# Optimization experiments

Hardware: AMD Instinct MI355X
Metric: run time of the kernel (lower is better)

## Reference

```python
import jax, jax.numpy as jnp
import numpy as np

B, Q, H, W, C = 2, 8192, 64, 64, 64
C9 = C * 9
EPS = 1e-6


def _mlp(x, params):
    # gelu MLP, no activation on last layer (matches repo mlp)
    for Wm, b in params[:-1]:
        x = jax.nn.gelu(x @ Wm + b)
    Wl, bl = params[-1]
    return x @ Wl + bl


def _make_coord(h, w):
    # pixel-center coords in (-1,1); channel 0 = row dim, channel 1 = col dim
    hs = -1.0 + (2.0 * jnp.arange(h, dtype=jnp.float32) + 1.0) / h
    ws = -1.0 + (2.0 * jnp.arange(w, dtype=jnp.float32) + 1.0) / w
    return jnp.stack(jnp.meshgrid(hs, ws, indexing='ij'), axis=0)  # (2,h,w)


def _nearest_gather(feat, coord):
    # F.grid_sample(mode='nearest', align_corners=False) on a (B,1,q,2) grid.
    # feat (B,C,H,W); coord (B,q,2) with [...,0] indexing H, [...,1] indexing W
    h, w = feat.shape[-2], feat.shape[-1]
    ih = jnp.clip(jnp.round((coord[..., 0] + 1.0) * h / 2.0 - 0.5), 0, h - 1).astype(jnp.int32)
    iw = jnp.clip(jnp.round((coord[..., 1] + 1.0) * w / 2.0 - 0.5), 0, w - 1).astype(jnp.int32)
    return jax.vmap(lambda f, a, b: f[:, a, b].T)(feat, ih, iw)  # (B,q,C)


def _unfold3(feat):
    # F.unfold(feat, 3, padding=1).view(B, C*9, H, W): channel-major, kernel row-major
    b, c, h, w = feat.shape
    p = jnp.pad(feat, ((0, 0), (0, 0), (1, 1), (1, 1)))
    patches = jnp.stack([p[:, :, i:i + h, j:j + w] for i in range(3) for j in range(3)], axis=2)
    return patches.reshape(b, c * 9, h, w)


def _forward(inp, coord, scale, enc_w, enc_b, iw0, ib0, iw1, ib1, iw2, ib2,
             sw0, sb0, sw1, sb1, ww0, wb0, ww1, wb1):
    # encoder (stand-in conv3x3, 3 -> C feature channels)
    feat = jax.lax.conv_general_dilated(inp, enc_w, (1, 1), 'SAME',
                                        dimension_numbers=('NCHW', 'OIHW', 'NCHW'))
    feat = feat + enc_b[None, :, None, None]
    feat = _unfold3(feat)  # (B, C*9, H, W)
    bsz, cf, h, w = feat.shape
    fcoord = jnp.broadcast_to(_make_coord(h, w)[None], (bsz, 2, h, w))
    dims = jnp.array([h, w], dtype=feat.dtype)

    tx = (h - 1) / (1.0 - scale[:, 0, 0])  # (B,)
    ty = (w - 1) / (1.0 - scale[:, 0, 1])
    rx, ry = 1.0 / tx, 1.0 / ty
    scale_tok = scale * dims  # (B,q,2)

    imnet_p = [(iw0, ib0), (iw1, ib1), (iw2, ib2)]
    score_p = [(sw0, sb0), (sw1, sb1)]
    weight_p = [(ww0, wb0), (ww1, wb1)]

    preds = []
    for vx in (-1, 1):
        for vy in (-1, 1):
            shift = jnp.stack([vx * rx + EPS, vy * ry + EPS], axis=-1)[:, None, :]  # (B,1,2)
            c = jnp.clip(coord + shift, -1.0 + 1e-6, 1.0 - 1e-6)
            value = _nearest_gather(feat, c)      # (B,q,C*9)
            coord_k = _nearest_gather(fcoord, c)  # (B,q,2)
            rel = (coord - coord_k) * dims        # (B,q,2)
            score = _mlp(rel, score_p)            # (B,q,1) -> broadcast over 3
            mlp_in = jnp.concatenate([rel, scale_tok], axis=-1)  # (B,q,4)
            wmat = _mlp(mlp_in, imnet_p).reshape(bsz, -1, cf, 3)  # (B,q,C*9,3)
            preds.append(jnp.einsum('bqc,bqck->bqk', value, wmat) + score)
    stacked = jnp.stack(preds, axis=-1)  # (B,q,3,4)
    return _mlp(stacked, weight_p)[..., 0]  # (B,q,3)


def setup_inputs() -> dict:
    key = jax.random.key(0)
    ks = jax.random.split(key, 16)
    f32 = jnp.float32

    def wi(k, shape, fan_in):
        return jax.random.normal(k, shape, f32) / np.float32(np.sqrt(fan_in))

    return {
        'inp': jax.random.normal(ks[0], (B, 3, H, W), f32),
        'coord': jax.random.uniform(ks[1], (B, Q, 2), f32, -1.0 + 1e-4, 1.0 - 1e-4),
        'scale': jax.random.uniform(ks[2], (B, Q, 2), f32, 0.01, 0.05),
        'enc_w': wi(ks[3], (C, 3, 3, 3), 27),
        'enc_b': jnp.zeros((C,), f32),
        'iw0': wi(ks[4], (4, 256), 4), 'ib0': jnp.zeros((256,), f32),
        'iw1': wi(ks[5], (256, 256), 256), 'ib1': jnp.zeros((256,), f32),
        'iw2': wi(ks[6], (256, C9 * 3), 256), 'ib2': jnp.zeros((C9 * 3,), f32),
        'sw0': wi(ks[7], (2, 256), 2), 'sb0': jnp.zeros((256,), f32),
        'sw1': wi(ks[8], (256, 1), 256), 'sb1': jnp.zeros((1,), f32),
        'ww0': wi(ks[9], (4, 256), 4), 'wb0': jnp.zeros((256,), f32),
        'ww1': wi(ks[10], (256, 1), 256), 'wb1': jnp.zeros((1,), f32),
    }


def reference(inp, coord, scale, enc_w, enc_b, iw0, ib0, iw1, ib1, iw2, ib2,
              sw0, sb0, sw1, sb1, ww0, wb0, ww1, wb1):
    return _forward(inp, coord, scale, enc_w, enc_b, iw0, ib0, iw1, ib1, iw2, ib2,
                    sw0, sb0, sw1, sb1, ww0, wb0, ww1, wb1)
```

## Files before the change

### kernel.cpp

```cpp
#include <hip/hip_runtime.h>

#define QN 8192
#define CCH 64
#define NROW 65536
#define MR 64
#define NBLK (NROW / MR)
#define H0S 264

typedef _Float16 f16x8 __attribute__((ext_vector_type(8)));
typedef _Float16 f16x4 __attribute__((ext_vector_type(4)));
typedef float f32x4 __attribute__((ext_vector_type(4)));

__device__ __forceinline__ float gelu_f(float x) {
    float x2 = x * x;
    float tt = fmaf(0.044715f, x2, 1.0f);
    float e = __expf(1.5957691216f * x * tt);
    float r = __builtin_amdgcn_rcpf(1.0f + e);
    return x - x * r;
}

__global__ __launch_bounds__(256) void k_pre(const float* __restrict__ inp,
                                             const float* __restrict__ ew,
                                             const float* __restrict__ eb,
                                             const float* __restrict__ coord,
                                             const float* __restrict__ scale,
                                             const float* __restrict__ sw0,
                                             const float* __restrict__ sb0,
                                             const float* __restrict__ sw1,
                                             const float* __restrict__ sb1,
                                             const float* __restrict__ iw1,
                                             const float* __restrict__ iw2,
                                             const float* __restrict__ ib2,
                                             float* __restrict__ featpad,
                                             float4* __restrict__ mlp_in,
                                             int2* __restrict__ ihiw,
                                             float* __restrict__ scoreg,
                                             _Float16* __restrict__ w1tp,
                                             _Float16* __restrict__ w2tp,
                                             float* __restrict__ b2p) {
    const int bb = blockIdx.x;
    const int tt0 = threadIdx.x;
    if (bb < 2178) {
        __shared__ float s_ew[1728];
        for (int i = tt0; i < 1728; i += 256) s_ew[i] = ew[i];
        __syncthreads();
        int idx = bb * 256 + tt0;
        const int total = 2 * 66 * 66 * CCH;
        if (idx >= total) return;
        int o = idx & 63; int pix = idx >> 6;
        int xx = pix % 66; int t2 = pix / 66;
        int yy = t2 % 66;  int b = t2 / 66;
        int y = yy - 1, x = xx - 1;
        float acc = 0.0f;
        if (y >= 0 && y < 64 && x >= 0 && x < 64) {
            acc = eb[o];
            for (int i = 0; i < 3; ++i) {
                const float* ip = inp + ((b * 3 + i) * 64) * 64;
                const float* wp = s_ew + (o * 3 + i) * 9;
                #pragma unroll
                for (int ky = 0; ky < 3; ++ky) {
                    int sy = y + ky - 1;
                    if (sy < 0 || sy > 63) continue;
                    #pragma unroll
                    for (int kx = 0; kx < 3; ++kx) {
                        int sx = x + kx - 1;
                        if (sx < 0 || sx > 63) continue;
                        acc += ip[sy * 64 + sx] * wp[ky * 3 + kx];
                    }
                }
            }
        }
        featpad[idx] = acc;
    } else if (bb < 2434) {
        int row = (bb - 2178) * 256 + tt0;
        int v = row & 3;
        int bq = row >> 2;
        int b = bq >> 13;
        float c0 = coord[bq * 2 + 0], c1 = coord[bq * 2 + 1];
        float s0 = scale[bq * 2 + 0], s1 = scale[bq * 2 + 1];
        float s00 = scale[(b * QN) * 2 + 0];
        float s01 = scale[(b * QN) * 2 + 1];
        float rx = (1.0f - s00) / 63.0f;
        float ry = (1.0f - s01) / 63.0f;
        float vx = (v & 2) ? 1.0f : -1.0f;
        float vy = (v & 1) ? 1.0f : -1.0f;
        float cc0 = c0 + vx * rx + 1e-6f;
        float cc1 = c1 + vy * ry + 1e-6f;
        cc0 = fminf(fmaxf(cc0, -1.0f + 1e-6f), 1.0f - 1e-6f);
        cc1 = fminf(fmaxf(cc1, -1.0f + 1e-6f), 1.0f - 1e-6f);
        int ih = (int)rintf((cc0 + 1.0f) * 32.0f - 0.5f);
        int iw = (int)rintf((cc1 + 1.0f) * 32.0f - 0.5f);
        ih = min(max(ih, 0), 63);
        iw = min(max(iw, 0), 63);
        float ck0 = (2.0f * (float)ih + 1.0f) / 64.0f - 1.0f;
        float ck1 = (2.0f * (float)iw + 1.0f) / 64.0f - 1.0f;
        float rel0 = (c0 - ck0) * 64.0f;
        float rel1 = (c1 - ck1) * 64.0f;
        mlp_in[row] = make_float4(rel0, rel1, s0 * 64.0f, s1 * 64.0f);
        ihiw[row] = make_int2(ih, iw);
        float sc = sb1[0];
        #pragma unroll 4
        for (int t2 = 0; t2 < 256; ++t2) {
            float h = gelu_f(fmaf(rel0, sw0[t2], fmaf(rel1, sw0[256 + t2], sb0[t2])));
            sc = fmaf(h, sw1[t2], sc);
        }
        scoreg[row] = sc;
    } else {
        int idx = (bb - 2434) * 256 + tt0;
        if (idx < 442368) {
            int j = idx & 7, ln = (idx >> 3) & 63, kf = (idx >> 9) & 7, tl = idx >> 12;
            int np = tl * 16 + (ln & 15);
            int kk = kf * 32 + (ln >> 4) * 8 + j;
            int k_out = np / 576;
            int rem = np - 576 * k_out;
            int tap = rem >> 6, cch = rem & 63;
            int n = (cch * 9 + tap) * 3 + k_out;
            w2tp[idx] = (_Float16)iw2[kk * 1728 + n];
            if (kf == 0 && j == 0 && (ln >> 4) == 0) b2p[np] = ib2[n];
        } else {
            int i2 = idx - 442368;
            int j = i2 & 7, ln = (i2 >> 3) & 63, kf = (i2 >> 9) & 7, ct = i2 >> 12;
            int col = ct * 16 + (ln & 15);
            int kk = kf * 32 + (ln >> 4) * 8 + j;
            w1tp[i2] = (_Float16)iw1[kk * 256 + col];
        }
    }
}

#define LDX1(B, CT) do { const _Float16* wp_ = w1tp + (size_t)((CT) * 8) * 512 + lane * 8;        \
    _Pragma("unroll") for (int kf_ = 0; kf_ < 4; ++kf_) B[kf_] = *(const f16x8*)(wp_ + kf_ * 512); } while (0)
#define LDY1(B, CT) do { const _Float16* wp_ = w1tp + (size_t)((CT) * 8 + 4) * 512 + lane * 8;    \
    _Pragma("unroll") for (int kf_ = 0; kf_ < 4; ++kf_) B[kf_] = *(const f16x8*)(wp_ + kf_ * 512); } while (0)
#define LDX2(B, TI) do { const _Float16* wp_ = w2tp + (size_t)((TI) * 8) * 512 + lane * 8;        \
    _Pragma("unroll") for (int kf_ = 0; kf_ < 4; ++kf_) B[kf_] = *(const f16x8*)(wp_ + kf_ * 512); } while (0)
#define LDY2(B, BV, TI) do { const _Float16* wp_ = w2tp + (size_t)((TI) * 8 + 4) * 512 + lane * 8;\
    _Pragma("unroll") for (int kf_ = 0; kf_ < 4; ++kf_) B[kf_] = *(const f16x8*)(wp_ + kf_ * 512);\
    BV = b2p[(TI) * 16 + l15]; } while (0)
#define ZACCB(BV) do { _Pragma("unroll") for (int rt_ = 0; rt_ < 4; ++rt_)                        \
    acc[rt_] = (f32x4){(BV), (BV), (BV), (BV)}; } while (0)
#define MFMAH(B, OFS) do { _Pragma("unroll") for (int kf_ = 0; kf_ < 4; ++kf_)                    \
    { _Pragma("unroll") for (int rt_ = 0; rt_ < 4; ++rt_)                                         \
      acc[rt_] = __builtin_amdgcn_mfma_f32_16x16x32_f16(a[rt_][kf_ + (OFS)], B[kf_], acc[rt_], 0, 0, 0); } } while (0)
#define H1EPI(CT) do { int col_ = (CT) * 16 + l15;                                                \
    _Pragma("unroll") for (int rt_ = 0; rt_ < 4; ++rt_)                                           \
      { _Pragma("unroll") for (int rg_ = 0; rg_ < 4; ++rg_)                                       \
        s_h0[(rt_ * 16 + quad * 4 + rg_) * H0S + col_] = (_Float16)gelu_f(acc[rt_][rg_]); } } while (0)
#define VLD(TI) do { int cf36_ = (TI) - ((TI) / 36) * 36;                                         \
    const _Float16* vb_ = s_valT + (cf36_ * 16 + l15) * 64;                                       \
    vv0 = *(const f16x4*)(vb_ + ((0  + quad * 4) ^ swz));                                         \
    vv1 = *(const f16x4*)(vb_ + ((16 + quad * 4) ^ swz));                                         \
    vv2 = *(const f16x4*)(vb_ + ((32 + quad * 4) ^ swz));                                         \
    vv3 = *(const f16x4*)(vb_ + ((48 + quad * 4) ^ swz)); } while (0)
#define EPIR(RT, VV) do { _Pragma("unroll") for (int rg_ = 0; rg_ < 4; ++rg_)                     \
    pA[RT][rg_] = fmaf(acc[RT][rg_], (float)VV[rg_], pA[RT][rg_]); } while (0)
#define EPI3F() do { EPIR(0, vv0); EPIR(1, vv1); EPIR(2, vv2); EPIR(3, vv3); } while (0)
#define FLUSH(KT) do { _Pragma("unroll") for (int rt_ = 0; rt_ < 4; ++rt_)                        \
    { _Pragma("unroll") for (int rg_ = 0; rg_ < 4; ++rg_) {                                       \
        float x_ = pA[rt_][rg_];                                                                  \
        _Pragma("unroll") for (int m_ = 1; m_ < 16; m_ <<= 1) x_ += __shfl_xor(x_, m_, 64);       \
        if (l15 == 0) atomicAdd(&s_pred[rt_ * 16 + quad * 4 + rg_][KT], x_);                      \
        pA[rt_][rg_] = 0.f; } } } while (0)

__global__ __launch_bounds__(256, 2) void k_fused(const float* __restrict__ featpad,
                                                  const float4* __restrict__ mlp_in,
                                                  const int2* __restrict__ ihiw,
                                                  const float* __restrict__ iw0,
                                                  const float* __restrict__ ib0,
                                                  const _Float16* __restrict__ w1tp,
                                                  const float* __restrict__ ib1,
                                                  const _Float16* __restrict__ w2tp,
                                                  const float* __restrict__ b2p,
                                                  const float* __restrict__ scoreg,
                                                  const float* __restrict__ ww0,
                                                  const float* __restrict__ wb0,
                                                  const float* __restrict__ ww1,
                                                  const float* __restrict__ wb1,
                                                  float* __restrict__ out) {
    __shared__ __align__(16) char pool[576 * 64 * 2];
    _Float16* s_h0   = (_Float16*)pool;
    _Float16* s_valT = (_Float16*)pool;
    __shared__ float4 s_min[MR];
    __shared__ int    s_base[MR];
    __shared__ int    s_dtab[9];
    __shared__ float  s_pred[MR][3];
    __shared__ float  s_score[MR];
    __shared__ float  s_wred[48][4];

    const int t = threadIdx.x;
    const int wave = t >> 6, lane = t & 63, quad = lane >> 4, l15 = lane & 15;
    const int rowbase = blockIdx.x * MR;

    if (t < MR) {
        int row = rowbase + t;
        s_min[t] = mlp_in[row];
        s_score[t] = scoreg[row];
        int b = row >> 15;
        int2 p = ihiw[row];
        s_base[t] = ((b * 66 + p.x) * 66 + p.y) * 64;
    }
    if (t < 9) { int di = t / 3; s_dtab[t] = (di * 66 + (t - 3 * di)) * 64; }
    if (t < MR * 3) s_pred[t / 3][t % 3] = 0.0f;
    __syncthreads();

    {
        float w0 = iw0[t], w1 = iw0[256 + t], w2 = iw0[512 + t], w3 = iw0[768 + t];
        float bb = ib0[t];
        #pragma unroll 4
        for (int r = 0; r < MR; ++r) {
            float4 m = s_min[r];
            s_h0[r * H0S + t] =
                (_Float16)gelu_f(fmaf(m.x, w0, fmaf(m.y, w1, fmaf(m.z, w2, fmaf(m.w, w3, bb)))));
        }
    }
    __syncthreads();

    const int w4 = wave * 4;
    const int tbase = wave * 27;

    const float bibA = ib1[(w4 + 0) * 16 + l15];
    const float bibB = ib1[(w4 + 1) * 16 + l15];
    const float bibC = ib1[(w4 + 2) * 16 + l15];
    const float bibD = ib1[(w4 + 3) * 16 + l15];

    f16x8 bX0[4], bX1[4], bY0[4], bY1[4];
    float bv0, bv1;
    f32x4 acc[4];

    LDX1(bX0, w4);
    LDY1(bY0, w4);
    LDX1(bX1, w4 + 1);

    f16x8 a[4][8];
    #pragma unroll
    for (int rt = 0; rt < 4; ++rt)
        #pragma unroll
        for (int kf = 0; kf < 8; ++kf)
            a[rt][kf] = *(const f16x8*)(s_h0 + (rt * 16 + l15) * H0S + kf * 32 + quad * 8);
    __syncthreads();

    LDY1(bY1, w4 + 1);
    ZACCB(bibA); MFMAH(bX0, 0);
    LDX1(bX0, w4 + 2);
    MFMAH(bY0, 4);
    H1EPI(w4);
    LDY1(bY0, w4 + 2);
    ZACCB(bibB); MFMAH(bX1, 0);
    LDX1(bX1, w4 + 3);
    MFMAH(bY1, 4);
    H1EPI(w4 + 1);
    LDY1(bY1, w4 + 3);
    ZACCB(bibC); MFMAH(bX0, 0);
    LDX2(bX0, tbase);
    MFMAH(bY0, 4);
    H1EPI(w4 + 2);
    LDY2(bY0, bv0, tbase);
    ZACCB(bibD); MFMAH(bX1, 0);
    LDX2(bX1, tbase + 1);
    MFMAH(bY1, 4);
    H1EPI(w4 + 3);
    __syncthreads();

    #pragma unroll
    for (int rt = 0; rt < 4; ++rt)
        #pragma unroll
        for (int kf = 0; kf < 8; ++kf)
            a[rt][kf] = *(const f16x8*)(s_h0 + (rt * 16 + l15) * H0S + kf * 32 + quad * 8);
    __syncthreads();

    #pragma unroll 1
    for (int g4 = 0; g4 < 9; ++g4) {
        float4 v[4];
        #pragma unroll
        for (int u = 0; u < 4; ++u) {
            int c4 = wave + (g4 * 4 + u) * 4;
            int tap = c4 >> 4;
            int cch0 = (c4 & 15) << 2;
            v[u] = *(const float4*)(featpad + s_base[lane] + s_dtab[tap] + cch0);
        }
        #pragma unroll
        for (int u = 0; u < 4; ++u) {
            int c4 = wave + (g4 * 4 + u) * 4;
            int cfp = c4 << 2;
            s_valT[(cfp + 0) * 64 + (lane ^ (((cfp + 0) & 7) << 3))] = (_Float16)v[u].x;
            s_valT[(cfp + 1) * 64 + (lane ^ (((cfp + 1) & 7) << 3))] = (_Float16)v[u].y;
            s_valT[(cfp + 2) * 64 + (lane ^ (((cfp + 2) & 7) << 3))] = (_Float16)v[u].z;
            s_valT[(cfp + 3) * 64 + (lane ^ (((cfp + 3) & 7) << 3))] = (_Float16)v[u].w;
        }
    }
    __syncthreads();

    const int kt0 = tbase / 36;
    int bsplit = (kt0 + 1) * 36 - tbase; if (bsplit > 27) bsplit = 27;
    const int ktB = (tbase + 26) / 36;
    const int swz = (l15 & 7) << 3;

    f16x4 vv0, vv1, vv2, vv3;
    float pA[4][4];
    #pragma unroll
    for (int rt = 0; rt < 4; ++rt)
        #pragma unroll
        for (int rg = 0; rg < 4; ++rg) pA[rt][rg] = 0.f;

    #pragma unroll 1
    for (int p = 0; p < 13; ++p) {
        int i = 2 * p;
        int ti = tbase + i;
        LDY2(bY1, bv1, ti + 1);
        VLD(ti);
        ZACCB(bv0); MFMAH(bX0, 0);
        LDX2(bX0, ti + 2);
        MFMAH(bY0, 4);
        EPI3F();
        if (i == bsplit - 1) FLUSH(kt0);
        LDY2(bY0, bv0, ti + 2);
        VLD(ti + 1);
        ZACCB(bv1); MFMAH(bX1, 0);
        if (p < 12) LDX2(bX1, ti + 3);
        MFMAH(bY1, 4);
        EPI3F();
        if (i + 1 == bsplit - 1) FLUSH(kt0);
    }
    {
        VLD(tbase + 26);
        ZACCB(bv0); MFMAH(bX0, 0); MFMAH(bY0, 4);
        EPI3F();
        if (26 == bsplit - 1) FLUSH(kt0);
    }
    FLUSH(ktB);
    __syncthreads();

    if (t < 192) {
        int o = t >> 2, sub = t & 3;
        int bql = o / 3, k = o - 3 * bql;
        float x0 = s_pred[bql * 4 + 0][k] + s_score[bql * 4 + 0];
        float x1 = s_pred[bql * 4 + 1][k] + s_score[bql * 4 + 1];
        float x2 = s_pred[bql * 4 + 2][k] + s_score[bql * 4 + 2];
        float x3 = s_pred[bql * 4 + 3][k] + s_score[bql * 4 + 3];
        float acc2 = 0.0f;
        int j0 = sub * 64;
        #pragma unroll 4
        for (int j = j0; j < j0 + 64; ++j) {
            float h = gelu_f(fmaf(x0, ww0[j], fmaf(x1, ww0[256 + j],
                          fmaf(x2, ww0[512 + j], fmaf(x3, ww0[768 + j], wb0[j])))));
            acc2 = fmaf(h, ww1[j], acc2);
        }
        s_wred[o][sub] = acc2;
    }
    __syncthreads();
    if (t < 48) {
        int bql = t / 3, k = t - 3 * bql;
        float r2 = s_wred[t][0] + s_wred[t][1] + s_wred[t][2] + s_wred[t][3] + wb1[0];
        out[(blockIdx.x * 16 + bql) * 3 + k] = r2;
    }
}

extern "C" void kernel_launch(void* const* d_in, const int* in_sizes, int n_in,
                              void* d_out, int out_size, void* d_ws, size_t ws_size,
                              hipStream_t stream) {
    const float* inp   = (const float*)d_in[0];
    const float* coord = (const float*)d_in[1];
    const float* scale = (const float*)d_in[2];
    const float* ew    = (const float*)d_in[3];
    const float* eb    = (const float*)d_in[4];
    const float* iw0   = (const float*)d_in[5];
    const float* ib0   = (const float*)d_in[6];
    const float* iw1   = (const float*)d_in[7];
    const float* ib1   = (const float*)d_in[8];
    const float* iw2   = (const float*)d_in[9];
    const float* ib2   = (const float*)d_in[10];
    const float* sw0   = (const float*)d_in[11];
    const float* sb0   = (const float*)d_in[12];
    const float* sw1   = (const float*)d_in[13];
    const float* sb1   = (const float*)d_in[14];
    const float* ww0   = (const float*)d_in[15];
    const float* wb0   = (const float*)d_in[16];
    const float* ww1   = (const float*)d_in[17];
    const float* wb1   = (const float*)d_in[18];
    float* out = (float*)d_out;

    char* ws = (char*)d_ws;
    float*     featpad = (float*)(ws + 0);
    float4*    mlp_in  = (float4*)(ws + 2230272);
    int2*      ihiw    = (int2*)(ws + 3278848);
    float*     scoreg  = (float*)(ws + 3803136);
    _Float16*  w1tp    = (_Float16*)(ws + 4065280);
    _Float16*  w2tp    = (_Float16*)(ws + 4196352);
    float*     b2p     = (float*)(ws + 5081088);

    k_pre<<<dim3(4418), dim3(256), 0, stream>>>(inp, ew, eb, coord, scale,
                                                sw0, sb0, sw1, sb1, iw1, iw2, ib2,
                                                featpad, mlp_in, ihiw, scoreg,
                                                w1tp, w2tp, b2p);
    k_fused<<<dim3(NBLK), dim3(256), 0, stream>>>(featpad, mlp_in, ihiw,
                                                  iw0, ib0, w1tp, ib1, w2tp, b2p,
                                                  scoreg, ww0, wb0, ww1, wb1, out);
}
```

Measured before the change: 240.7 us.

## Software-pipeline feature gather, raise MFMA wave priority, use exp2 in gelu

Replaces the 9-iteration gather loop with a double-buffered sequence of 8-wide float4 loads into two register sets, so global loads overlap the LDS transpose stores. The first gather batch is also issued before the A-fragment reload. Each MFMA burst is wrapped in s_setprio so waves issuing matrix ops get scheduling priority over epilogue waves. The value reads from s_valT move from before the MFMAs to inside the epilogue, which shortens register live ranges. gelu now calls the native exp2 with a folded log2(e) constant. The cost is more registers for the 16 float4 buffers, which could hurt occupancy at launch_bounds(256,2).

```diff
diff --git a/kernel.cpp b/kernel.cpp
--- a/kernel.cpp
+++ b/kernel.cpp
@@ -14,7 +14,7 @@
 __device__ __forceinline__ float gelu_f(float x) {
     float x2 = x * x;
     float tt = fmaf(0.044715f, x2, 1.0f);
-    float e = __expf(1.5957691216f * x * tt);
+    float e = __builtin_amdgcn_exp2f(2.3022081597f * x * tt);
     float r = __builtin_amdgcn_rcpf(1.0f + e);
     return x - x * r;
 }
@@ -145,21 +145,31 @@
     _Pragma("unroll") for (int rt_ = 0; rt_ < 4; ++rt_)                                           \
       { _Pragma("unroll") for (int rg_ = 0; rg_ < 4; ++rg_)                                       \
         s_h0[(rt_ * 16 + quad * 4 + rg_) * H0S + col_] = (_Float16)gelu_f(acc[rt_][rg_]); } } while (0)
-#define VLD(TI) do { int cf36_ = (TI) - ((TI) / 36) * 36;                                         \
+#define EPI3(TI) do { int cf36_ = (TI) - ((TI) / 36) * 36;                                        \
     const _Float16* vb_ = s_valT + (cf36_ * 16 + l15) * 64;                                       \
-    vv0 = *(const f16x4*)(vb_ + ((0  + quad * 4) ^ swz));                                         \
-    vv1 = *(const f16x4*)(vb_ + ((16 + quad * 4) ^ swz));                                         \
-    vv2 = *(const f16x4*)(vb_ + ((32 + quad * 4) ^ swz));                                         \
-    vv3 = *(const f16x4*)(vb_ + ((48 + quad * 4) ^ swz)); } while (0)
-#define EPIR(RT, VV) do { _Pragma("unroll") for (int rg_ = 0; rg_ < 4; ++rg_)                     \
-    pA[RT][rg_] = fmaf(acc[RT][rg_], (float)VV[rg_], pA[RT][rg_]); } while (0)
-#define EPI3F() do { EPIR(0, vv0); EPIR(1, vv1); EPIR(2, vv2); EPIR(3, vv3); } while (0)
+    _Pragma("unroll") for (int rt_ = 0; rt_ < 4; ++rt_) {                                         \
+      f16x4 vv_ = *(const f16x4*)(vb_ + ((rt_ * 16 + quad * 4) ^ swz));                           \
+      _Pragma("unroll") for (int rg_ = 0; rg_ < 4; ++rg_)                                         \
+        pA[rt_][rg_] = fmaf(acc[rt_][rg_], (float)vv_[rg_], pA[rt_][rg_]); } } while (0)
 #define FLUSH(KT) do { _Pragma("unroll") for (int rt_ = 0; rt_ < 4; ++rt_)                        \
     { _Pragma("unroll") for (int rg_ = 0; rg_ < 4; ++rg_) {                                       \
         float x_ = pA[rt_][rg_];                                                                  \
         _Pragma("unroll") for (int m_ = 1; m_ < 16; m_ <<= 1) x_ += __shfl_xor(x_, m_, 64);       \
         if (l15 == 0) atomicAdd(&s_pred[rt_ * 16 + quad * 4 + rg_][KT], x_);                      \
         pA[rt_][rg_] = 0.f; } } } while (0)
+
+#define GLDN(V, B, N) do { _Pragma("unroll") for (int u_ = 0; u_ < (N); ++u_) {                   \
+    int c4_ = wave + ((B) * 8 + u_) * 4;                                                          \
+    int tap_ = c4_ >> 4; int cch0_ = (c4_ & 15) << 2;                                             \
+    V[u_] = *(const float4*)(featpad + gbase + s_dtab[tap_] + cch0_); } } while (0)
+#define GSTN(V, B, N) do { _Pragma("unroll") for (int u_ = 0; u_ < (N); ++u_) {                   \
+    int c4_ = wave + ((B) * 8 + u_) * 4;                                                          \
+    int cfp_ = c4_ << 2;                                                                          \
+    s_valT[(cfp_ + 0) * 64 + (lane ^ (((cfp_ + 0) & 7) << 3))] = (_Float16)V[u_].x;               \
+    s_valT[(cfp_ + 1) * 64 + (lane ^ (((cfp_ + 1) & 7) << 3))] = (_Float16)V[u_].y;               \
+    s_valT[(cfp_ + 2) * 64 + (lane ^ (((cfp_ + 2) & 7) << 3))] = (_Float16)V[u_].z;               \
+    s_valT[(cfp_ + 3) * 64 + (lane ^ (((cfp_ + 3) & 7) << 3))] = (_Float16)V[u_].w;               \
+    } } while (0)
 
 __global__ __launch_bounds__(256, 2) void k_fused(const float* __restrict__ featpad,
                                                   const float4* __restrict__ mlp_in,
@@ -239,26 +249,37 @@
     __syncthreads();
 
     LDY1(bY1, w4 + 1);
+    __builtin_amdgcn_s_setprio(1);
     ZACCB(bibA); MFMAH(bX0, 0);
     LDX1(bX0, w4 + 2);
     MFMAH(bY0, 4);
+    __builtin_amdgcn_s_setprio(0);
     H1EPI(w4);
     LDY1(bY0, w4 + 2);
+    __builtin_amdgcn_s_setprio(1);
     ZACCB(bibB); MFMAH(bX1, 0);
     LDX1(bX1, w4 + 3);
     MFMAH(bY1, 4);
+    __builtin_amdgcn_s_setprio(0);
     H1EPI(w4 + 1);
     LDY1(bY1, w4 + 3);
+    __builtin_amdgcn_s_setprio(1);
     ZACCB(bibC); MFMAH(bX0, 0);
     LDX2(bX0, tbase);
     MFMAH(bY0, 4);
+    __builtin_amdgcn_s_setprio(0);
     H1EPI(w4 + 2);
     LDY2(bY0, bv0, tbase);
+    __builtin_amdgcn_s_setprio(1);
     ZACCB(bibD); MFMAH(bX1, 0);
-    LDX2(bX1, tbase + 1);
     MFMAH(bY1, 4);
+    __builtin_amdgcn_s_setprio(0);
     H1EPI(w4 + 3);
     __syncthreads();
+
+    float4 gv[8], gw[8];
+    const int gbase = s_base[lane];
+    GLDN(gv, 0, 8);
 
     #pragma unroll
     for (int rt = 0; rt < 4; ++rt)
@@ -267,26 +288,16 @@
             a[rt][kf] = *(const f16x8*)(s_h0 + (rt * 16 + l15) * H0S + kf * 32 + quad * 8);
     __syncthreads();
 
-    #pragma unroll 1
-    for (int g4 = 0; g4 < 9; ++g4) {
-        float4 v[4];
-        #pragma unroll
-        for (int u = 0; u < 4; ++u) {
-            int c4 = wave + (g4 * 4 + u) * 4;
-            int tap = c4 >> 4;
-            int cch0 = (c4 & 15) << 2;
-            v[u] = *(const float4*)(featpad + s_base[lane] + s_dtab[tap] + cch0);
-        }
-        #pragma unroll
-        for (int u = 0; u < 4; ++u) {
-            int c4 = wave + (g4 * 4 + u) * 4;
-            int cfp = c4 << 2;
-            s_valT[(cfp + 0) * 64 + (lane ^ (((cfp + 0) & 7) << 3))] = (_Float16)v[u].x;
-            s_valT[(cfp + 1) * 64 + (lane ^ (((cfp + 1) & 7) << 3))] = (_Float16)v[u].y;
-            s_valT[(cfp + 2) * 64 + (lane ^ (((cfp + 2) & 7) << 3))] = (_Float16)v[u].z;
-            s_valT[(cfp + 3) * 64 + (lane ^ (((cfp + 3) & 7) << 3))] = (_Float16)v[u].w;
-        }
-    }
+    GLDN(gw, 1, 8);
+    GSTN(gv, 0, 8);
+    GLDN(gv, 2, 8);
+    GSTN(gw, 1, 8);
+    GLDN(gw, 3, 8);
+    GSTN(gv, 2, 8);
+    GLDN(gv, 4, 4);
+    GSTN(gw, 3, 8);
+    GSTN(gv, 4, 4);
+    LDX2(bX1, tbase + 1);
     __syncthreads();
 
     const int kt0 = tbase / 36;
@@ -294,7 +305,6 @@
     const int ktB = (tbase + 26) / 36;
     const int swz = (l15 & 7) << 3;
 
-    f16x4 vv0, vv1, vv2, vv3;
     float pA[4][4];
     #pragma unroll
     for (int rt = 0; rt < 4; ++rt)
@@ -306,24 +316,27 @@
         int i = 2 * p;
         int ti = tbase + i;
         LDY2(bY1, bv1, ti + 1);
-        VLD(ti);
+        __builtin_amdgcn_s_setprio(1);
         ZACCB(bv0); MFMAH(bX0, 0);
         LDX2(bX0, ti + 2);
         MFMAH(bY0, 4);
-        EPI3F();
+        __builtin_amdgcn_s_setprio(0);
+        EPI3(ti);
         if (i == bsplit - 1) FLUSH(kt0);
         LDY2(bY0, bv0, ti + 2);
-        VLD(ti + 1);
+        __builtin_amdgcn_s_setprio(1);
         ZACCB(bv1); MFMAH(bX1, 0);
         if (p < 12) LDX2(bX1, ti + 3);
         MFMAH(bY1, 4);
-        EPI3F();
+        __builtin_amdgcn_s_setprio(0);
+        EPI3(ti + 1);
         if (i + 1 == bsplit - 1) FLUSH(kt0);
     }
     {
-        VLD(tbase + 26);
+        __builtin_amdgcn_s_setprio(1);
         ZACCB(bv0); MFMAH(bX0, 0); MFMAH(bY0, 4);
-        EPI3F();
+        __builtin_amdgcn_s_setprio(0);
+        EPI3(tbase + 26);
         if (26 == bsplit - 1) FLUSH(kt0);
     }
     FLUSH(ktB);
```

Result: faster. 232.6 us (-3.4%).

## Precompute per-pixel projection of last imnet layer onto unfolded features

Applied to the files above, without the earlier changes.

Reassociates the final imnet layer with the per-pixel feature dot product. A new kernel computes, for each of the 8192 feature pixels, the product of the 576-wide unfolded feature vector with W2 (and the bias) into a 784-wide fp16 table. The per-query kernel then needs only a 256-wide dot product of the hidden activation against the gathered table row, instead of a 256x1728 GEMM per query. This trades a large per-query MFMA workload for a smaller per-pixel GEMM, an extra launch and an intermediate buffer with fp16 rounding. GELU also switches to exp2 with a prescaled constant.

```diff
diff --git a/kernel.cpp b/kernel.cpp
--- a/kernel.cpp
+++ b/kernel.cpp
@@ -6,6 +6,8 @@
 #define MR 64
 #define NBLK (NROW / MR)
 #define H0S 264
+#define UW 784
+#define SVP 592
 
 typedef _Float16 f16x8 __attribute__((ext_vector_type(8)));
 typedef _Float16 f16x4 __attribute__((ext_vector_type(4)));
@@ -14,7 +16,7 @@
 __device__ __forceinline__ float gelu_f(float x) {
     float x2 = x * x;
     float tt = fmaf(0.044715f, x2, 1.0f);
-    float e = __expf(1.5957691216f * x * tt);
+    float e = __builtin_amdgcn_exp2f(2.3022081597f * x * tt);
     float r = __builtin_amdgcn_rcpf(1.0f + e);
     return x - x * r;
 }
@@ -36,8 +38,7 @@
                                              int2* __restrict__ ihiw,
                                              float* __restrict__ scoreg,
                                              _Float16* __restrict__ w1tp,
-                                             _Float16* __restrict__ w2tp,
-                                             float* __restrict__ b2p) {
+                                             _Float16* __restrict__ w3tp) {
     const int bb = blockIdx.x;
     const int tt0 = threadIdx.x;
     if (bb < 2178) {
@@ -107,18 +108,23 @@
         scoreg[row] = sc;
     } else {
         int idx = (bb - 2434) * 256 + tt0;
-        if (idx < 442368) {
-            int j = idx & 7, ln = (idx >> 3) & 63, kf = (idx >> 9) & 7, tl = idx >> 12;
-            int np = tl * 16 + (ln & 15);
-            int kk = kf * 32 + (ln >> 4) * 8 + j;
-            int k_out = np / 576;
-            int rem = np - 576 * k_out;
-            int tap = rem >> 6, cch = rem & 63;
-            int n = (cch * 9 + tap) * 3 + k_out;
-            w2tp[idx] = (_Float16)iw2[kk * 1728 + n];
-            if (kf == 0 && j == 0 && (ln >> 4) == 0) b2p[np] = ib2[n];
+        if (idx < 451584) {
+            int jj = idx & 7, ln = (idx >> 3) & 63;
+            int tlkf = idx >> 9;
+            int tl = tlkf / 18, kf = tlkf - tl * 18;
+            int o = tl * 16 + (ln & 15);
+            int v = kf * 32 + (ln >> 4) * 8 + jj;
+            int tap = v >> 6, cch = v & 63;
+            float val = 0.0f;
+            if (o < 768) {
+                int j = o & 255, k = o >> 8;
+                val = iw2[j * 1728 + (cch * 9 + tap) * 3 + k];
+            } else if (o < 771) {
+                val = ib2[(cch * 9 + tap) * 3 + (o - 768)];
+            }
+            w3tp[idx] = (_Float16)val;
         } else {
-            int i2 = idx - 442368;
+            int i2 = idx - 451584;
             int j = i2 & 7, ln = (i2 >> 3) & 63, kf = (i2 >> 9) & 7, ct = i2 >> 12;
             int col = ct * 16 + (ln & 15);
             int kk = kf * 32 + (ln >> 4) * 8 + j;
@@ -127,15 +133,61 @@
     }
 }
 
+__global__ __launch_bounds__(256) void k_u(const float* __restrict__ featpad,
+                                           const _Float16* __restrict__ w3tp,
+                                           _Float16* __restrict__ u) {
+    __shared__ __align__(16) _Float16 s_val[32 * SVP];
+    __shared__ int s_dtab[9];
+    const int t = threadIdx.x;
+    const int wave = t >> 6, lane = t & 63, quad = lane >> 4, l15 = lane & 15;
+    if (t < 9) { int dy = t / 3; s_dtab[t] = (dy * 66 + (t - 3 * dy)) * 64; }
+    {
+        int p = t & 31, half = t >> 5;
+        int slot = blockIdx.x * 32 + p;
+        int b = slot >> 12, rem = slot & 4095, y = rem >> 6, x = rem & 63;
+        int base = ((b * 66 + y) * 66 + x) * 64;
+        __syncthreads();
+        #pragma unroll
+        for (int i = 0; i < 18; ++i) {
+            int v0 = half * 72 + i * 4;
+            int tap = v0 >> 6, cch = v0 & 63;
+            float4 f = *(const float4*)(featpad + base + s_dtab[tap] + cch);
+            f16x4 hv = {(_Float16)f.x, (_Float16)f.y, (_Float16)f.z, (_Float16)f.w};
+            *(f16x4*)(s_val + p * SVP + v0) = hv;
+        }
+    }
+    __syncthreads();
+
+    const int t0 = (wave == 0) ? 0 : 1 + wave * 12;
+    const int nt = (wave == 0) ? 13 : 12;
+    #pragma unroll 1
+    for (int tt = 0; tt < nt; ++tt) {
+        int tl = t0 + tt;
+        const _Float16* wp = w3tp + ((size_t)(tl * 18) * 64 + lane) * 8;
+        f16x8 bbuf[18];
+        #pragma unroll
+        for (int kf = 0; kf < 18; ++kf) bbuf[kf] = *(const f16x8*)(wp + (size_t)kf * 512);
+        f32x4 ac0 = {0.f, 0.f, 0.f, 0.f}, ac1 = {0.f, 0.f, 0.f, 0.f};
+        #pragma unroll
+        for (int kf = 0; kf < 18; ++kf) {
+            f16x8 a0 = *(const f16x8*)(s_val + l15 * SVP + kf * 32 + quad * 8);
+            f16x8 a1 = *(const f16x8*)(s_val + (16 + l15) * SVP + kf * 32 + quad * 8);
+            ac0 = __builtin_amdgcn_mfma_f32_16x16x32_f16(a0, bbuf[kf], ac0, 0, 0, 0);
+            ac1 = __builtin_amdgcn_mfma_f32_16x16x32_f16(a1, bbuf[kf], ac1, 0, 0, 0);
+        }
+        size_t pb = (size_t)(blockIdx.x * 32 + quad * 4) * UW + tl * 16 + l15;
+        #pragma unroll
+        for (int rg = 0; rg < 4; ++rg) u[pb + (size_t)rg * UW] = (_Float16)ac0[rg];
+        pb += (size_t)16 * UW;
+        #pragma unroll
+        for (int rg = 0; rg < 4; ++rg) u[pb + (size_t)rg * UW] = (_Float16)ac1[rg];
+    }
+}
+
 #define LDX1(B, CT) do { const _Float16* wp_ = w1tp + (size_t)((CT) * 8) * 512 + lane * 8;        \
     _Pragma("unroll") for (int kf_ = 0; kf_ < 4; ++kf_) B[kf_] = *(const f16x8*)(wp_ + kf_ * 512); } while (0)
 #define LDY1(B, CT) do { const _Float16* wp_ = w1tp + (size_t)((CT) * 8 + 4) * 512 + lane * 8;    \
     _Pragma("unroll") for (int kf_ = 0; kf_ < 4; ++kf_) B[kf_] = *(const f16x8*)(wp_ + kf_ * 512); } while (0)
-#define LDX2(B, TI) do { const _Float16* wp_ = w2tp + (size_t)((TI) * 8) * 512 + lane * 8;        \
-    _Pragma("unroll") for (int kf_ = 0; kf_ < 4; ++kf_) B[kf_] = *(const f16x8*)(wp_ + kf_ * 512); } while (0)
-#define LDY2(B, BV, TI) do { const _Float16* wp_ = w2tp + (size_t)((TI) * 8 + 4) * 512 + lane * 8;\
-    _Pragma("unroll") for (int kf_ = 0; kf_ < 4; ++kf_) B[kf_] = *(const f16x8*)(wp_ + kf_ * 512);\
-    BV = b2p[(TI) * 16 + l15]; } while (0)
 #define ZACCB(BV) do { _Pragma("unroll") for (int rt_ = 0; rt_ < 4; ++rt_)                        \
     acc[rt_] = (f32x4){(BV), (BV), (BV), (BV)}; } while (0)
 #define MFMAH(B, OFS) do { _Pragma("unroll") for (int kf_ = 0; kf_ < 4; ++kf_)                    \
@@ -145,45 +197,26 @@
     _Pragma("unroll") for (int rt_ = 0; rt_ < 4; ++rt_)                                           \
       { _Pragma("unroll") for (int rg_ = 0; rg_ < 4; ++rg_)                                       \
         s_h0[(rt_ * 16 + quad * 4 + rg_) * H0S + col_] = (_Float16)gelu_f(acc[rt_][rg_]); } } while (0)
-#define VLD(TI) do { int cf36_ = (TI) - ((TI) / 36) * 36;                                         \
-    const _Float16* vb_ = s_valT + (cf36_ * 16 + l15) * 64;                                       \
-    vv0 = *(const f16x4*)(vb_ + ((0  + quad * 4) ^ swz));                                         \
-    vv1 = *(const f16x4*)(vb_ + ((16 + quad * 4) ^ swz));                                         \
-    vv2 = *(const f16x4*)(vb_ + ((32 + quad * 4) ^ swz));                                         \
-    vv3 = *(const f16x4*)(vb_ + ((48 + quad * 4) ^ swz)); } while (0)
-#define EPIR(RT, VV) do { _Pragma("unroll") for (int rg_ = 0; rg_ < 4; ++rg_)                     \
-    pA[RT][rg_] = fmaf(acc[RT][rg_], (float)VV[rg_], pA[RT][rg_]); } while (0)
-#define EPI3F() do { EPIR(0, vv0); EPIR(1, vv1); EPIR(2, vv2); EPIR(3, vv3); } while (0)
-#define FLUSH(KT) do { _Pragma("unroll") for (int rt_ = 0; rt_ < 4; ++rt_)                        \
-    { _Pragma("unroll") for (int rg_ = 0; rg_ < 4; ++rg_) {                                       \
-        float x_ = pA[rt_][rg_];                                                                  \
-        _Pragma("unroll") for (int m_ = 1; m_ < 16; m_ <<= 1) x_ += __shfl_xor(x_, m_, 64);       \
-        if (l15 == 0) atomicAdd(&s_pred[rt_ * 16 + quad * 4 + rg_][KT], x_);                      \
-        pA[rt_][rg_] = 0.f; } } } while (0)
-
-__global__ __launch_bounds__(256, 2) void k_fused(const float* __restrict__ featpad,
-                                                  const float4* __restrict__ mlp_in,
-                                                  const int2* __restrict__ ihiw,
-                                                  const float* __restrict__ iw0,
-                                                  const float* __restrict__ ib0,
-                                                  const _Float16* __restrict__ w1tp,
-                                                  const float* __restrict__ ib1,
-                                                  const _Float16* __restrict__ w2tp,
-                                                  const float* __restrict__ b2p,
-                                                  const float* __restrict__ scoreg,
-                                                  const float* __restrict__ ww0,
-                                                  const float* __restrict__ wb0,
-                                                  const float* __restrict__ ww1,
-                                                  const float* __restrict__ wb1,
-                                                  float* __restrict__ out) {
-    __shared__ __align__(16) char pool[576 * 64 * 2];
-    _Float16* s_h0   = (_Float16*)pool;
-    _Float16* s_valT = (_Float16*)pool;
+
+__global__ __launch_bounds__(256, 2) void k_dot(const float4* __restrict__ mlp_in,
+                                                const int2* __restrict__ ihiw,
+                                                const float* __restrict__ iw0,
+                                                const float* __restrict__ ib0,
+                                                const _Float16* __restrict__ w1tp,
+                                                const float* __restrict__ ib1,
+                                                const _Float16* __restrict__ ubuf,
+                                                const float* __restrict__ scoreg,
+                                                const float* __restrict__ ww0,
+                                                const float* __restrict__ wb0,
+                                                const float* __restrict__ ww1,
+                                                const float* __restrict__ wb1,
+                                                float* __restrict__ out) {
+    __shared__ __align__(16) _Float16 s_h0[MR * H0S];
     __shared__ float4 s_min[MR];
-    __shared__ int    s_base[MR];
-    __shared__ int    s_dtab[9];
+    __shared__ int    s_slot[MR];
     __shared__ float  s_pred[MR][3];
     __shared__ float  s_score[MR];
+    __shared__ float  s_dred[MR][3][4];
     __shared__ float  s_wred[48][4];
 
     const int t = threadIdx.x;
@@ -196,10 +229,8 @@
         s_score[t] = scoreg[row];
         int b = row >> 15;
         int2 p = ihiw[row];
-        s_base[t] = ((b * 66 + p.x) * 66 + p.y) * 64;
-    }
-    if (t < 9) { int di = t / 3; s_dtab[t] = (di * 66 + (t - 3 * di)) * 64; }
-    if (t < MR * 3) s_pred[t / 3][t % 3] = 0.0f;
+        s_slot[t] = (b << 12) + (p.x << 6) + p.y;
+    }
     __syncthreads();
 
     {
@@ -215,15 +246,12 @@
     __syncthreads();
 
     const int w4 = wave * 4;
-    const int tbase = wave * 27;
-
     const float bibA = ib1[(w4 + 0) * 16 + l15];
     const float bibB = ib1[(w4 + 1) * 16 + l15];
     const float bibC = ib1[(w4 + 2) * 16 + l15];
     const float bibD = ib1[(w4 + 3) * 16 + l15];
 
     f16x8 bX0[4], bX1[4], bY0[4], bY1[4];
-    float bv0, bv1;
     f32x4 acc[4];
 
     LDX1(bX0, w4);
@@ -250,83 +278,48 @@
     H1EPI(w4 + 1);
     LDY1(bY1, w4 + 3);
     ZACCB(bibC); MFMAH(bX0, 0);
-    LDX2(bX0, tbase);
     MFMAH(bY0, 4);
     H1EPI(w4 + 2);
-    LDY2(bY0, bv0, tbase);
     ZACCB(bibD); MFMAH(bX1, 0);
-    LDX2(bX1, tbase + 1);
     MFMAH(bY1, 4);
     H1EPI(w4 + 3);
     __syncthreads();
 
-    #pragma unroll
-    for (int rt = 0; rt < 4; ++rt)
-        #pragma unroll
-        for (int kf = 0; kf < 8; ++kf)
-            a[rt][kf] = *(const f16x8*)(s_h0 + (rt * 16 + l15) * H0S + kf * 32 + quad * 8);
-    __syncthreads();
-
-    #pragma unroll 1
-    for (int g4 = 0; g4 < 9; ++g4) {
-        float4 v[4];
-        #pragma unroll
-        for (int u = 0; u < 4; ++u) {
-            int c4 = wave + (g4 * 4 + u) * 4;
-            int tap = c4 >> 4;
-            int cch0 = (c4 & 15) << 2;
-            v[u] = *(const float4*)(featpad + s_base[lane] + s_dtab[tap] + cch0);
-        }
-        #pragma unroll
-        for (int u = 0; u < 4; ++u) {
-            int c4 = wave + (g4 * 4 + u) * 4;
-            int cfp = c4 << 2;
-            s_valT[(cfp + 0) * 64 + (lane ^ (((cfp + 0) & 7) << 3))] = (_Float16)v[u].x;
-            s_valT[(cfp + 1) * 64 + (lane ^ (((cfp + 1) & 7) << 3))] = (_Float16)v[u].y;
-            s_valT[(cfp + 2) * 64 + (lane ^ (((cfp + 2) & 7) << 3))] = (_Float16)v[u].z;
-            s_valT[(cfp + 3) * 64 + (lane ^ (((cfp + 3) & 7) << 3))] = (_Float16)v[u].w;
-        }
-    }
-    __syncthreads();
-
-    const int kt0 = tbase / 36;
-    int bsplit = (kt0 + 1) * 36 - tbase; if (bsplit > 27) bsplit = 27;
-    const int ktB = (tbase + 26) / 36;
-    const int swz = (l15 & 7) << 3;
-
-    f16x4 vv0, vv1, vv2, vv3;
-    float pA[4][4];
-    #pragma unroll
-    for (int rt = 0; rt < 4; ++rt)
-        #pragma unroll
-        for (int rg = 0; rg < 4; ++rg) pA[rt][rg] = 0.f;
-
-    #pragma unroll 1
-    for (int p = 0; p < 13; ++p) {
-        int i = 2 * p;
-        int ti = tbase + i;
-        LDY2(bY1, bv1, ti + 1);
-        VLD(ti);
-        ZACCB(bv0); MFMAH(bX0, 0);
-        LDX2(bX0, ti + 2);
-        MFMAH(bY0, 4);
-        EPI3F();
-        if (i == bsplit - 1) FLUSH(kt0);
-        LDY2(bY0, bv0, ti + 2);
-        VLD(ti + 1);
-        ZACCB(bv1); MFMAH(bX1, 0);
-        if (p < 12) LDX2(bX1, ti + 3);
-        MFMAH(bY1, 4);
-        EPI3F();
-        if (i + 1 == bsplit - 1) FLUSH(kt0);
-    }
     {
-        VLD(tbase + 26);
-        ZACCB(bv0); MFMAH(bX0, 0); MFMAH(bY0, 4);
-        EPI3F();
-        if (26 == bsplit - 1) FLUSH(kt0);
-    }
-    FLUSH(ktB);
+        int r = t >> 2, sub = t & 3;
+        int j0 = sub * 64;
+        size_t sb = (size_t)s_slot[r] * UW;
+        float a0 = 0.f, a1 = 0.f, a2 = 0.f;
+        #pragma unroll
+        for (int g = 0; g < 4; ++g) {
+            int j = j0 + g * 16;
+            f16x8 hA  = *(const f16x8*)(s_h0 + r * H0S + j);
+            f16x8 hB  = *(const f16x8*)(s_h0 + r * H0S + j + 8);
+            f16x8 u0A = *(const f16x8*)(ubuf + sb + j);
+            f16x8 u0B = *(const f16x8*)(ubuf + sb + j + 8);
+            f16x8 u1A = *(const f16x8*)(ubuf + sb + 256 + j);
+            f16x8 u1B = *(const f16x8*)(ubuf + sb + 256 + j + 8);
+            f16x8 u2A = *(const f16x8*)(ubuf + sb + 512 + j);
+            f16x8 u2B = *(const f16x8*)(ubuf + sb + 512 + j + 8);
+            #pragma unroll
+            for (int e = 0; e < 8; ++e) {
+                float hx = (float)hA[e], hy = (float)hB[e];
+                a0 = fmaf(hx, (float)u0A[e], a0); a0 = fmaf(hy, (float)u0B[e], a0);
+                a1 = fmaf(hx, (float)u1A[e], a1); a1 = fmaf(hy, (float)u1B[e], a1);
+                a2 = fmaf(hx, (float)u2A[e], a2); a2 = fmaf(hy, (float)u2B[e], a2);
+            }
+        }
+        s_dred[r][0][sub] = a0;
+        s_dred[r][1][sub] = a1;
+        s_dred[r][2][sub] = a2;
+    }
+    __syncthreads();
+    if (t < 192) {
+        int r = t / 3, k = t - 3 * r;
+        float s = s_dred[r][k][0] + s_dred[r][k][1] + s_dred[r][k][2] + s_dred[r][k][3]
+                + (float)ubuf[(size_t)s_slot[r] * UW + 768 + k];
+        s_pred[r][k] = s;
+    }
     __syncthreads();
 
     if (t < 192) {
@@ -384,14 +377,14 @@
     int2*      ihiw    = (int2*)(ws + 3278848);
     float*     scoreg  = (float*)(ws + 3803136);
     _Float16*  w1tp    = (_Float16*)(ws + 4065280);
-    _Float16*  w2tp    = (_Float16*)(ws + 4196352);
-    float*     b2p     = (float*)(ws + 5081088);
-
-    k_pre<<<dim3(4418), dim3(256), 0, stream>>>(inp, ew, eb, coord, scale,
+    _Float16*  w3tp    = (_Float16*)(ws + 4196352);
+    _Float16*  u       = (_Float16*)(ws + 5099520);
+
+    k_pre<<<dim3(4454), dim3(256), 0, stream>>>(inp, ew, eb, coord, scale,
                                                 sw0, sb0, sw1, sb1, iw1, iw2, ib2,
                                                 featpad, mlp_in, ihiw, scoreg,
-                                                w1tp, w2tp, b2p);
-    k_fused<<<dim3(NBLK), dim3(256), 0, stream>>>(featpad, mlp_in, ihiw,
-                                                  iw0, ib0, w1tp, ib1, w2tp, b2p,
-                                                  scoreg, ww0, wb0, ww1, wb1, out);
-}
+                                                w1tp, w3tp);
+    k_u<<<dim3(256), dim3(256), 0, stream>>>(featpad, w3tp, u);
+    k_dot<<<dim3(NBLK), dim3(256), 0, stream>>>(mlp_in, ihiw, iw0, ib0, w1tp, ib1,
+                                                u, scoreg, ww0, wb0, ww1, wb1, out);
+}
```

Measured after the change: 224.5 us. 1.07x faster.
